# Kernel optimization log

Measured on AMD Instinct MI355X. Metric: run time of the kernel, lower is better.

Reference implementation:

```python
import jax, jax.numpy as jnp
import numpy as np

B, S, D, H, KS, VS, O = 4, 2048, 1024, 16, 64, 64, 1024


def setup_inputs() -> dict:
    key = jax.random.key(0)
    ks = jax.random.split(key, 11)
    def w(k, shp):
        return jax.random.normal(k, shp, dtype=jnp.float32) * 0.02
    return {
        "Q": jax.random.normal(ks[0], (B, S, D), dtype=jnp.float32),
        "K": jax.random.normal(ks[1], (B, S, D), dtype=jnp.float32),
        "V": jax.random.normal(ks[2], (B, S, D), dtype=jnp.float32),
        # per-head projection weights stacked over heads (equivalent to 3*H separate nn.Linear)
        "Wq": w(ks[3], (H, D, KS)), "bq": w(ks[4], (H, KS)),
        "Wk": w(ks[5], (H, D, KS)), "bk": w(ks[6], (H, KS)),
        "Wv": w(ks[7], (H, D, VS)), "bv": w(ks[8], (H, VS)),
        "Wo": w(ks[9], (H * VS, O)), "bo": w(ks[10], (O,)),
    }


def reference(Q, K, V, Wq, bq, Wk, bk, Wv, bv, Wo, bo):
    scale = jnp.sqrt(jnp.asarray(KS, dtype=Q.dtype))
    # per-head linear projections (vectorized over heads)
    q = jnp.einsum('bsd,hdk->bhsk', Q, Wq) + bq[:, None, :]   # [B,H,S,KS]
    k = jnp.einsum('bsd,hdk->bhsk', K, Wk) + bk[:, None, :]   # [B,H,S,KS]
    v = jnp.einsum('bsd,hdv->bhsv', V, Wv) + bv[:, None, :]   # [B,H,S,VS]
    # scaled dot-product attention, full S x S scores per head
    scores = jnp.einsum('bhsk,bhtk->bhst', q, k) / scale       # [B,H,S,S]
    attn = jax.nn.softmax(scores, axis=-1)
    heads = jnp.einsum('bhst,bhtv->bhsv', attn, v)             # [B,H,S,VS]
    # concat heads along feature dim -> [B,S,H*VS]
    cat = jnp.transpose(heads, (0, 2, 1, 3)).reshape(B, S, H * VS)
    return cat @ Wo + bo
```

## Files before the change

kernel.cpp:

```cpp
#include <hip/hip_runtime.h>
#include <hip/hip_fp16.h>
#include <cstdint>
#include <cstddef>

typedef _Float16 f16;
typedef _Float16 f16x8 __attribute__((ext_vector_type(8)));
typedef _Float16 f16x4 __attribute__((ext_vector_type(4)));
typedef float    f32x4 __attribute__((ext_vector_type(4)));

#define MFMA(a, b, c) __builtin_amdgcn_mfma_f32_16x16x32_f16(a, b, c, 0, 0, 0)


__device__ __forceinline__ void gload_lds16(const f16* g, f16* l) {
    __builtin_amdgcn_global_load_lds(
        (const __attribute__((address_space(1))) void*)g,
        (__attribute__((address_space(3))) void*)l, 16, 0, 0);
}

__global__ void k_transpose_all(const float* __restrict__ Wq, const float* __restrict__ Wk,
                                const float* __restrict__ Wv, const float* __restrict__ Wo,
                                f16* __restrict__ WT, f16* __restrict__ WoT) {
    __shared__ float T[64][65];
    const int bx = blockIdx.x;
    const int widx = bx >> 8, sub = bx & 255;
    const int nb = sub >> 4, db = sub & 15;
    const int tid = threadIdx.x;
    const float* W = widx == 0 ? Wq : (widx == 1 ? Wk : (widx == 2 ? Wv : Wo));
    f16* Wt = (widx < 3) ? (WT + (size_t)widx * 1048576) : WoT;
    const float* src = (widx < 3) ? (W + nb * 65536 + db * 4096)
                                  : (W + db * 65536 + nb * 64);
    const int rstride = (widx < 3) ? 64 : 1024;
    {
        int nn = tid & 63, d0 = tid >> 6;
#pragma unroll
        for (int p = 0; p < 16; ++p) {
            int dd = p * 4 + d0;
            T[dd][nn] = src[dd * rstride + nn];
        }
    }
    __syncthreads();
    {
        int dd = tid & 63, n0 = tid >> 6;
#pragma unroll
        for (int p = 0; p < 16; ++p) {
            int nn = p * 4 + n0;
            Wt[(size_t)(nb * 64 + nn) * 1024 + db * 64 + dd] = (f16)T[dd][nn];
        }
    }
}

#define G256_STAGE(AD, BD, ASRC, BSRC, KT)                                      \
    do {                                                                        \
        int ktc = (KT);                                                         \
        _Pragma("unroll")                                                       \
        for (int i2 = 0; i2 < 4; ++i2) {                                        \
            int gA = wid * 4 + i2;                                              \
            gload_lds16(&(ASRC)[(size_t)(row0 + gA * 8 + (lane >> 3)) * 1024    \
                                + ktc * 64 + (lane & 7) * 8],                   \
                        &(AD)[(gA * 68 + lane) * 8]);                           \
        }                                                                       \
        _Pragma("unroll")                                                       \
        for (int i2 = 0; i2 < 2; ++i2) {                                        \
            int gB = wid * 2 + i2;                                              \
            gload_lds16(&(BSRC)[(size_t)(col0 + gB * 8 + (lane >> 3)) * 1024    \
                                + ktc * 64 + (lane & 7) * 8],                   \
                        &(BD)[(gB * 68 + lane) * 8]);                           \
        }                                                                       \
    } while (0)

#define G256_STAGE_B(BD, BSRC, KT)                                             \
    do {                                                                        \
        int ktc = (KT);                                                         \
        _Pragma("unroll")                                                       \
        for (int i2 = 0; i2 < 2; ++i2) {                                        \
            int gB = wid * 2 + i2;                                              \
            gload_lds16(&(BSRC)[(size_t)(col0 + gB * 8 + (lane >> 3)) * 1024    \
                                + ktc * 64 + (lane & 7) * 8],                   \
                        &(BD)[(gB * 68 + lane) * 8]);                           \
        }                                                                       \
    } while (0)

#define QKV_ISSUE_A(KT)                                                         \
    do {                                                                        \
        int ktc = (KT);                                                         \
        _Pragma("unroll")                                                       \
        for (int i2 = 0; i2 < 4; ++i2) {                                        \
            int gA = wid * 4 + i2;                                              \
            const float* p = &Af[(size_t)(row0 + gA * 8 + (lane >> 3)) * 1024   \
                                 + ktc * 64 + (lane & 7) * 8];                  \
            alo[i2] = *(const float4*)p;                                        \
            ahi[i2] = *(const float4*)(p + 4);                                  \
        }                                                                       \
    } while (0)

#define QKV_WRITE_A(AD)                                                         \
    do {                                                                        \
        _Pragma("unroll")                                                       \
        for (int i2 = 0; i2 < 4; ++i2) {                                        \
            int gA = wid * 4 + i2;                                              \
            union { uint32_t u[4]; f16x8 v; } hh;                               \
            hh.u[0] = __builtin_bit_cast(uint32_t,                              \
                        __builtin_amdgcn_cvt_pkrtz(alo[i2].x, alo[i2].y));      \
            hh.u[1] = __builtin_bit_cast(uint32_t,                              \
                        __builtin_amdgcn_cvt_pkrtz(alo[i2].z, alo[i2].w));      \
            hh.u[2] = __builtin_bit_cast(uint32_t,                              \
                        __builtin_amdgcn_cvt_pkrtz(ahi[i2].x, ahi[i2].y));      \
            hh.u[3] = __builtin_bit_cast(uint32_t,                              \
                        __builtin_amdgcn_cvt_pkrtz(ahi[i2].z, ahi[i2].w));      \
            *(f16x8*)&(AD)[(gA * 68 + lane) * 8] = hh.v;                        \
        }                                                                       \
    } while (0)

#define G256_COMPUTE(AB, BB)                                                    \
    do {                                                                        \
        _Pragma("unroll")                                                       \
        for (int kk = 0; kk < 2; ++kk) {                                        \
            f16x8 af[4], bf[4];                                                 \
            _Pragma("unroll")                                                   \
            for (int m = 0; m < 4; ++m) {                                       \
                int rw = wm * 64 + m * 16 + lr;                                 \
                af[m] = *(const f16x8*)&(AB)[((rw >> 3) * 68 + (rw & 7) * 8     \
                                              + kk * 4 + lg) * 8];              \
            }                                                                   \
            _Pragma("unroll")                                                   \
            for (int n = 0; n < 4; ++n) {                                       \
                int rw = wn * 64 + n * 16 + lr;                                 \
                bf[n] = *(const f16x8*)&(BB)[((rw >> 3) * 68 + (rw & 7) * 8     \
                                              + kk * 4 + lg) * 8];              \
            }                                                                   \
            _Pragma("unroll")                                                   \
            for (int m = 0; m < 4; ++m)                                         \
                _Pragma("unroll")                                               \
                for (int n = 0; n < 4; ++n)                                     \
                    acc[m][n] = MFMA(af[m], bf[n], acc[m][n]);                  \
        }                                                                       \
    } while (0)

#define G256_PIPELINE(ASRC, BSRC)                                              \
    int cur = 0, nx1 = 1, nx2 = 2;                                             \
    G256_STAGE(As3, Bs3, ASRC, BSRC, 0);                                       \
    for (int t = 0; t < 16; ++t) {                                             \
        int tn = t < 15 ? t + 1 : 15;                                          \
        G256_STAGE(As3 + nx1 * 17408, Bs3 + nx1 * 8704, ASRC, BSRC, tn);       \
        asm volatile("s_waitcnt vmcnt(6)" ::: "memory");                       \
        __builtin_amdgcn_sched_barrier(0);                                     \
        __builtin_amdgcn_s_barrier();                                          \
        __builtin_amdgcn_sched_barrier(0);                                     \
        const f16* Ab = As3 + cur * 17408;                                     \
        const f16* Bb = Bs3 + cur * 8704;                                      \
        G256_COMPUTE(Ab, Bb);                                                  \
        int tmp = cur; cur = nx1; nx1 = nx2; nx2 = tmp;                        \
    }

__global__ __launch_bounds__(512, 1) void k_gemm_qkv256(
    const float* __restrict__ Qf, const float* __restrict__ Kf, const float* __restrict__ Vf,
    const f16* __restrict__ WT, const float* __restrict__ bq,
    const float* __restrict__ bk, const float* __restrict__ bv,
    f16* __restrict__ qout, f16* __restrict__ kout, f16* __restrict__ vout, float SC) {
    __shared__ f16 As3[3 * 17408];
    __shared__ f16 Bs3[3 * 8704];
    const int yy = blockIdx.y;
    const int seg = yy >> 3;
    const float* Af = seg == 0 ? Qf : (seg == 1 ? Kf : Vf);
    const f16* Bt   = WT + (size_t)seg * 1048576;
    const float* bias = seg == 0 ? bq : (seg == 1 ? bk : bv);
    const float scale = seg == 0 ? SC : 1.0f;

    const int tid = threadIdx.x;
    const int wid = tid >> 6, lane = tid & 63;
    const int wm = wid >> 1, wn = wid & 1;
    const int lr = lane & 15, lg = lane >> 4;
    const int row0 = blockIdx.x * 256, col0 = (yy & 7) * 128;

    f32x4 acc[4][4];
#pragma unroll
    for (int m = 0; m < 4; ++m)
#pragma unroll
        for (int n = 0; n < 4; ++n) acc[m][n] = (f32x4){0.f, 0.f, 0.f, 0.f};

    float4 alo[4], ahi[4];

    G256_STAGE_B(Bs3, Bt, 0);
    QKV_ISSUE_A(0);
    asm volatile("s_waitcnt vmcnt(0)" ::: "memory");
    QKV_WRITE_A(As3);
    G256_STAGE_B(Bs3 + 8704, Bt, 1);
    QKV_ISSUE_A(1);
    asm volatile("s_waitcnt lgkmcnt(0)" ::: "memory");
    __builtin_amdgcn_sched_barrier(0);
    __builtin_amdgcn_s_barrier();
    __builtin_amdgcn_sched_barrier(0);

    int cur = 0, nx1 = 1, nx2 = 2;
    for (int t = 0; t < 16; ++t) {
        const f16* Ab = As3 + cur * 17408;
        const f16* Bb = Bs3 + cur * 8704;
        G256_COMPUTE(Ab, Bb);
        int tn2 = t + 2 <= 15 ? t + 2 : 15;
        asm volatile("s_waitcnt vmcnt(0)" ::: "memory");
        __builtin_amdgcn_sched_barrier(0);
        QKV_WRITE_A(As3 + nx1 * 17408);
        G256_STAGE_B(Bs3 + nx2 * 8704, Bt, tn2);
        QKV_ISSUE_A(tn2);
        asm volatile("s_waitcnt lgkmcnt(0)" ::: "memory");
        __builtin_amdgcn_sched_barrier(0);
        __builtin_amdgcn_s_barrier();
        __builtin_amdgcn_sched_barrier(0);
        int tmp = cur; cur = nx1; nx1 = nx2; nx2 = tmp;
    }

#pragma unroll
    for (int m = 0; m < 4; ++m) {
#pragma unroll
        for (int n = 0; n < 4; ++n) {
            int col = col0 + wn * 64 + n * 16 + lr;
            float bv_ = bias[col];
            int rowb = row0 + wm * 64 + m * 16 + lg * 4;
            int srow = rowb & 2047;
            if (seg == 0) {
#pragma unroll
                for (int r = 0; r < 4; ++r) {
                    int row = rowb + r;
                    size_t a = ((size_t)((row >> 11) * 16 + (col >> 6)) * 2048 + (row & 2047)) * 64 + (col & 63);
                    qout[a] = (f16)((acc[m][n][r] + bv_) * scale);
                }
            } else if (seg == 1) {
                int ks5 = srow & 31;
                int p0 = ((ks5 >> 2) & 1) * 16 + (ks5 >> 3) * 4 + (ks5 & 3);
                size_t abase = (size_t)((rowb >> 11) * 16 + (col >> 6)) * 131072
                             + (size_t)(srow >> 5) * 2048
                             + (size_t)(p0 >> 4) * 512
                             + (size_t)((col & 63) >> 5) * 1024
                             + (size_t)((col & 31) >> 3) * 128
                             + (col & 7);
#pragma unroll
                for (int r = 0; r < 4; ++r)
                    kout[abase + (size_t)((p0 & 15) + r) * 8] = (f16)(acc[m][n][r] + bv_);
            } else {
                size_t a = (size_t)((rowb >> 11) * 16 + (col >> 6)) * 131072
                         + (size_t)(srow >> 5) * 2048
                         + (size_t)((col & 63) >> 4) * 512
                         + (size_t)((srow & 31) >> 3) * 128
                         + (size_t)(col & 15) * 8
                         + (srow & 7);
                f16x4 ov;
#pragma unroll
                for (int r = 0; r < 4; ++r) ov[r] = (f16)(acc[m][n][r] + bv_);
                *(f16x4*)&vout[a] = ov;
            }
        }
    }
}

__global__ __launch_bounds__(512, 1) void k_gemm_out256(const f16* __restrict__ A,
                                                        const f16* __restrict__ Bt,
                                                        const float* __restrict__ bias,
                                                        float* __restrict__ Cout) {
    __shared__ f16 As3[3 * 17408];
    __shared__ f16 Bs3[3 * 8704];
    const int tid = threadIdx.x;
    const int wid = tid >> 6, lane = tid & 63;
    const int wm = wid >> 1, wn = wid & 1;
    const int lr = lane & 15, lg = lane >> 4;
    const int row0 = blockIdx.x * 256, col0 = blockIdx.y * 128;

    f32x4 acc[4][4];
#pragma unroll
    for (int m = 0; m < 4; ++m)
#pragma unroll
        for (int n = 0; n < 4; ++n) acc[m][n] = (f32x4){0.f, 0.f, 0.f, 0.f};

    G256_PIPELINE(A, Bt)

#pragma unroll
    for (int m = 0; m < 4; ++m) {
#pragma unroll
        for (int n = 0; n < 4; ++n) {
            int col = col0 + wn * 64 + n * 16 + lr;
            float bv = bias[col];
#pragma unroll
            for (int r = 0; r < 4; ++r) {
                int row = row0 + wm * 64 + m * 16 + lg * 4 + r;
                Cout[(size_t)row * 1024 + col] = acc[m][n][r] + bv;
            }
        }
    }
}

#define ATTN_TILE(Kc, Vc)                                                     \
    do {                                                                      \
        f16x8 ka0 = *(const f16x8*)&(Kc)[fo];                                 \
        f16x8 ka1 = *(const f16x8*)&(Kc)[fo + 1024];                          \
        f16x8 ka2 = *(const f16x8*)&(Kc)[fo + 512];                           \
        f16x8 ka3 = *(const f16x8*)&(Kc)[fo + 1536];                          \
        f32x4 st[2][2];                                                       \
        __builtin_amdgcn_s_setprio(1);                                        \
        _Pragma("unroll")                                                     \
        for (int qt = 0; qt < 2; ++qt) {                                      \
            float nm = -m_r[qt];                                              \
            f32x4 z = (f32x4){nm, nm, nm, nm};                                \
            z = MFMA(ka0, qf[qt][0], z);                                      \
            z = MFMA(ka1, qf[qt][1], z);                                      \
            st[qt][0] = z;                                                    \
            f32x4 z2 = (f32x4){nm, nm, nm, nm};                               \
            z2 = MFMA(ka2, qf[qt][0], z2);                                    \
            z2 = MFMA(ka3, qf[qt][1], z2);                                    \
            st[qt][1] = z2;                                                   \
        }                                                                     \
        __builtin_amdgcn_s_setprio(0);                                        \
        f16x8 vv0 = *(const f16x8*)&(Vc)[fo];                                 \
        f16x8 vv1 = *(const f16x8*)&(Vc)[fo + 512];                           \
        f16x8 vv2 = *(const f16x8*)&(Vc)[fo + 1024];                          \
        f16x8 vv3 = *(const f16x8*)&(Vc)[fo + 1536];                          \
        {                                                                     \
            float lm[2];                                                      \
            _Pragma("unroll")                                                 \
            for (int qt = 0; qt < 2; ++qt) {                                  \
                float a0 = fmaxf(fmaxf(st[qt][0][0], st[qt][0][1]), st[qt][0][2]); \
                float b0 = fmaxf(fmaxf(st[qt][0][3], st[qt][1][0]), st[qt][1][1]); \
                float c0 = fmaxf(fmaxf(st[qt][1][2], st[qt][1][3]), a0);      \
                lm[qt] = fmaxf(b0, c0);                                       \
            }                                                                 \
            if (__any((lm[0] > THR) || (lm[1] > THR))) {                      \
                _Pragma("unroll")                                             \
                for (int qt = 0; qt < 2; ++qt) {                              \
                    float t0v = lm[qt];                                       \
                    t0v = fmaxf(t0v, __shfl_xor(t0v, 16, 64));                \
                    t0v = fmaxf(t0v, __shfl_xor(t0v, 32, 64));                \
                    float delta = fmaxf(0.f, t0v);                            \
                    float alpha = __builtin_amdgcn_exp2f(-delta);             \
                    _Pragma("unroll")                                         \
                    for (int m = 0; m < 4; ++m)                               \
                        _Pragma("unroll")                                     \
                        for (int r = 0; r < 4; ++r) o[qt][m][r] *= alpha;     \
                    _Pragma("unroll")                                         \
                    for (int r = 0; r < 4; ++r) ol[qt][r] *= alpha;           \
                    m_r[qt] += delta;                                         \
                    _Pragma("unroll")                                         \
                    for (int t = 0; t < 2; ++t)                               \
                        _Pragma("unroll")                                     \
                        for (int r = 0; r < 4; ++r) st[qt][t][r] -= delta;    \
                }                                                             \
            }                                                                 \
        }                                                                     \
        f16x8 pf[2];                                                          \
        _Pragma("unroll")                                                     \
        for (int qt = 0; qt < 2; ++qt) {                                      \
            union { uint32_t u[4]; f16x8 v; } bb;                             \
            _Pragma("unroll")                                                 \
            for (int t = 0; t < 2; ++t)                                       \
                _Pragma("unroll")                                             \
                for (int pr = 0; pr < 2; ++pr) {                              \
                    float e0 = __builtin_amdgcn_exp2f(st[qt][t][2 * pr]);     \
                    float e1 = __builtin_amdgcn_exp2f(st[qt][t][2 * pr + 1]); \
                    auto hp = __builtin_amdgcn_cvt_pkrtz(e0, e1);             \
                    bb.u[t * 2 + pr] = __builtin_bit_cast(uint32_t, hp);      \
                }                                                             \
            pf[qt] = bb.v;                                                    \
        }                                                                     \
        __builtin_amdgcn_s_setprio(1);                                        \
        _Pragma("unroll")                                                     \
        for (int qt = 0; qt < 2; ++qt) {                                      \
            o[qt][0] = MFMA(vv0, pf[qt], o[qt][0]);                           \
            o[qt][1] = MFMA(vv1, pf[qt], o[qt][1]);                           \
            o[qt][2] = MFMA(vv2, pf[qt], o[qt][2]);                           \
            o[qt][3] = MFMA(vv3, pf[qt], o[qt][3]);                           \
            ol[qt]   = MFMA(ones, pf[qt], ol[qt]);                            \
        }                                                                     \
        __builtin_amdgcn_s_setprio(0);                                        \
    } while (0)

__global__ __launch_bounds__(512, 4) void k_attn(const f16* __restrict__ q,
                                                 const f16* __restrict__ k2,
                                                 const f16* __restrict__ v2,
                                                 f16* __restrict__ cat) {
    const int g = blockIdx.x;
    const int xcd = g & 7, i = g >> 3;
    const int bh = xcd * 8 + (i >> 3);
    const int qb = i & 7;
    const int b = bh >> 4, h = bh & 15;

    const int tid = threadIdx.x, wid = tid >> 6, lane = tid & 63;
    const int lr = lane & 15, lg = lane >> 4;
    const int qw = qb * 256 + wid * 32;

    __shared__ f16 Ks[4][2048];
    __shared__ f16 Vs[4][2048];

    const float THR = 8.0f;

    f16x8 qf[2][2];
#pragma unroll
    for (int qt = 0; qt < 2; ++qt)
#pragma unroll
        for (int hf = 0; hf < 2; ++hf)
            qf[qt][hf] = *(const f16x8*)&q[((size_t)bh * 2048 + qw + qt * 16 + lr) * 64 + hf * 32 + lg * 8];

    const f16* kt = k2 + (size_t)bh * 131072;
    const f16* vt = v2 + (size_t)bh * 131072;
    const bool sgK = (tid < 256);
    const int so2 = (tid & 255) * 8;
    const int fo = lane * 8;

    f16x8 ones;
#pragma unroll
    for (int j = 0; j < 8; ++j) ones[j] = (f16)1.0f;

    f32x4 o[2][4], ol[2];
#pragma unroll
    for (int qt = 0; qt < 2; ++qt) {
#pragma unroll
        for (int m = 0; m < 4; ++m) o[qt][m] = (f32x4){0.f, 0.f, 0.f, 0.f};
        ol[qt] = (f32x4){0.f, 0.f, 0.f, 0.f};
    }
    float m_r[2] = {0.f, 0.f};

    if (sgK) {
        gload_lds16(kt + so2, &Ks[0][so2]);
        gload_lds16(kt + 2048 + so2, &Ks[1][so2]);
    } else {
        gload_lds16(vt + so2, &Vs[0][so2]);
        gload_lds16(vt + 2048 + so2, &Vs[1][so2]);
    }
    __syncthreads();

    const bool rev = (wid & 1);
    for (int pp = 0; pp < 32; ++pp) {
        const int t0 = 2 * pp;
        const int ba = t0 & 3, bb2 = (t0 + 1) & 3;
        const int bc = (t0 + 2) & 3, bd = (t0 + 3) & 3;

        if (sgK) {
            gload_lds16(kt + (size_t)(t0 + 2) * 2048 + so2, &Ks[bc][so2]);
            gload_lds16(kt + (size_t)(t0 + 3) * 2048 + so2, &Ks[bd][so2]);
        } else {
            gload_lds16(vt + (size_t)(t0 + 2) * 2048 + so2, &Vs[bc][so2]);
            gload_lds16(vt + (size_t)(t0 + 3) * 2048 + so2, &Vs[bd][so2]);
        }

        if (rev) {
            ATTN_TILE(&Ks[bb2][0], &Vs[bb2][0]);
            ATTN_TILE(&Ks[ba][0], &Vs[ba][0]);
        } else {
            ATTN_TILE(&Ks[ba][0], &Vs[ba][0]);
            ATTN_TILE(&Ks[bb2][0], &Vs[bb2][0]);
        }

        __syncthreads();
    }

#pragma unroll
    for (int qt = 0; qt < 2; ++qt) {
        float inv = 1.f / ol[qt][0];
        size_t cb = ((size_t)b * 2048 + qw + qt * 16 + lr) * 1024 + h * 64 + lg * 4;
#pragma unroll
        for (int m = 0; m < 4; ++m) {
            f16x4 ov;
#pragma unroll
            for (int r = 0; r < 4; ++r) ov[r] = (f16)(o[qt][m][r] * inv);
            *(f16x4*)&cat[cb + m * 16] = ov;
        }
    }
}

extern "C" void kernel_launch(void* const* d_in, const int* in_sizes, int n_in,
                              void* d_out, int out_size, void* d_ws, size_t ws_size,
                              hipStream_t stream) {
    const float* Q  = (const float*)d_in[0];
    const float* K  = (const float*)d_in[1];
    const float* V  = (const float*)d_in[2];
    const float* Wq = (const float*)d_in[3];
    const float* bq = (const float*)d_in[4];
    const float* Wk = (const float*)d_in[5];
    const float* bk = (const float*)d_in[6];
    const float* Wv = (const float*)d_in[7];
    const float* bv = (const float*)d_in[8];
    const float* Wo = (const float*)d_in[9];
    const float* bo = (const float*)d_in[10];

    char* ws = (char*)d_ws;
    size_t off = 0;
    auto alloc = [&](size_t bytes) {
        char* p = ws + off;
        off += (bytes + 255) & ~(size_t)255;
        return p;
    };
    f16* WT  = (f16*)alloc(3ULL * 1024 * 1024 * 2);
    f16* WoT = (f16*)alloc(1024ULL * 1024 * 2);
    f16* qb  = (f16*)alloc(8192ULL * 1024 * 2);
    f16* kb2 = (f16*)alloc(8192ULL * 1024 * 2);
    f16* vb2 = (f16*)alloc(8192ULL * 1024 * 2);
    f16* cat = (f16*)alloc(8192ULL * 1024 * 2);

    k_transpose_all<<<1024, 256, 0, stream>>>(Wq, Wk, Wv, Wo, WT, WoT);

    const float SC = 0.125f * 1.44269504089f;
    k_gemm_qkv256<<<dim3(32, 24), 512, 0, stream>>>(Q, K, V, WT, bq, bk, bv,
                                                    qb, kb2, vb2, SC);

    k_attn<<<512, 512, 0, stream>>>(qb, kb2, vb2, cat);

    k_gemm_out256<<<dim3(32, 8), 512, 0, stream>>>(cat, WoT, bo, (float*)d_out);
}
```

Baseline: 183.4 us.

## Double-buffer A registers in QKV GEMM to keep loads in flight

Restructures the QKV projection main loop into a two-step unrolled pipeline with two register sets for the fp32 A tile. Each step issues the next tile's global loads, then uses a partial vmcnt wait so only the older loads must finish before converting and writing the current A tile to LDS. The previous loop waited on vmcnt(0) every iteration. The change aims to hide global load latency behind LDS writes and MFMA compute, at the cost of extra VGPRs for the second A buffer, which may lower occupancy. It also depends on the hand-counted vmcnt value being correct.

```diff
diff --git a/kernel.cpp b/kernel.cpp
--- a/kernel.cpp
+++ b/kernel.cpp
@@ -80,7 +80,7 @@
         }                                                                       \
     } while (0)
 
-#define QKV_ISSUE_A(KT)                                                         \
+#define QKV_ISSUE_A(ALO, AHI, KT)                                               \
     do {                                                                        \
         int ktc = (KT);                                                         \
         _Pragma("unroll")                                                       \
@@ -88,25 +88,25 @@
             int gA = wid * 4 + i2;                                              \
             const float* p = &Af[(size_t)(row0 + gA * 8 + (lane >> 3)) * 1024   \
                                  + ktc * 64 + (lane & 7) * 8];                  \
-            alo[i2] = *(const float4*)p;                                        \
-            ahi[i2] = *(const float4*)(p + 4);                                  \
+            ALO[i2] = *(const float4*)p;                                        \
+            AHI[i2] = *(const float4*)(p + 4);                                  \
         }                                                                       \
     } while (0)
 
-#define QKV_WRITE_A(AD)                                                         \
+#define QKV_WRITE_A(AD, ALO, AHI)                                               \
     do {                                                                        \
         _Pragma("unroll")                                                       \
         for (int i2 = 0; i2 < 4; ++i2) {                                        \
             int gA = wid * 4 + i2;                                              \
             union { uint32_t u[4]; f16x8 v; } hh;                               \
             hh.u[0] = __builtin_bit_cast(uint32_t,                              \
-                        __builtin_amdgcn_cvt_pkrtz(alo[i2].x, alo[i2].y));      \
+                        __builtin_amdgcn_cvt_pkrtz(ALO[i2].x, ALO[i2].y));      \
             hh.u[1] = __builtin_bit_cast(uint32_t,                              \
-                        __builtin_amdgcn_cvt_pkrtz(alo[i2].z, alo[i2].w));      \
+                        __builtin_amdgcn_cvt_pkrtz(ALO[i2].z, ALO[i2].w));      \
             hh.u[2] = __builtin_bit_cast(uint32_t,                              \
-                        __builtin_amdgcn_cvt_pkrtz(ahi[i2].x, ahi[i2].y));      \
+                        __builtin_amdgcn_cvt_pkrtz(AHI[i2].x, AHI[i2].y));      \
             hh.u[3] = __builtin_bit_cast(uint32_t,                              \
-                        __builtin_amdgcn_cvt_pkrtz(ahi[i2].z, ahi[i2].w));      \
+                        __builtin_amdgcn_cvt_pkrtz(AHI[i2].z, AHI[i2].w));      \
             *(f16x8*)&(AD)[(gA * 68 + lane) * 8] = hh.v;                        \
         }                                                                       \
     } while (0)
@@ -178,35 +178,45 @@
 #pragma unroll
         for (int n = 0; n < 4; ++n) acc[m][n] = (f32x4){0.f, 0.f, 0.f, 0.f};
 
-    float4 alo[4], ahi[4];
+    float4 aloA[4], ahiA[4], aloB[4], ahiB[4];
 
     G256_STAGE_B(Bs3, Bt, 0);
-    QKV_ISSUE_A(0);
-    asm volatile("s_waitcnt vmcnt(0)" ::: "memory");
-    QKV_WRITE_A(As3);
-    G256_STAGE_B(Bs3 + 8704, Bt, 1);
-    QKV_ISSUE_A(1);
-    asm volatile("s_waitcnt lgkmcnt(0)" ::: "memory");
-    __builtin_amdgcn_sched_barrier(0);
-    __builtin_amdgcn_s_barrier();
-    __builtin_amdgcn_sched_barrier(0);
+    QKV_ISSUE_A(aloA, ahiA, 0);
 
     int cur = 0, nx1 = 1, nx2 = 2;
-    for (int t = 0; t < 16; ++t) {
-        const f16* Ab = As3 + cur * 17408;
-        const f16* Bb = Bs3 + cur * 8704;
-        G256_COMPUTE(Ab, Bb);
-        int tn2 = t + 2 <= 15 ? t + 2 : 15;
-        asm volatile("s_waitcnt vmcnt(0)" ::: "memory");
-        __builtin_amdgcn_sched_barrier(0);
-        QKV_WRITE_A(As3 + nx1 * 17408);
-        G256_STAGE_B(Bs3 + nx2 * 8704, Bt, tn2);
-        QKV_ISSUE_A(tn2);
-        asm volatile("s_waitcnt lgkmcnt(0)" ::: "memory");
-        __builtin_amdgcn_sched_barrier(0);
-        __builtin_amdgcn_s_barrier();
-        __builtin_amdgcn_sched_barrier(0);
-        int tmp = cur; cur = nx1; nx1 = nx2; nx2 = tmp;
+    for (int tp = 0; tp < 8; ++tp) {
+        const int t0 = 2 * tp;
+        {
+            G256_STAGE_B(Bs3 + nx1 * 8704, Bt, t0 + 1);
+            QKV_ISSUE_A(aloB, ahiB, t0 + 1);
+            asm volatile("s_waitcnt vmcnt(10)" ::: "memory");
+            __builtin_amdgcn_sched_barrier(0);
+            QKV_WRITE_A(As3 + cur * 17408, aloA, ahiA);
+            asm volatile("s_waitcnt lgkmcnt(0)" ::: "memory");
+            __builtin_amdgcn_sched_barrier(0);
+            __builtin_amdgcn_s_barrier();
+            __builtin_amdgcn_sched_barrier(0);
+            G256_COMPUTE(As3 + cur * 17408, Bs3 + cur * 8704);
+            int tmp = cur; cur = nx1; nx1 = nx2; nx2 = tmp;
+        }
+        {
+            const int t1 = t0 + 1;
+            if (t1 < 15) {
+                G256_STAGE_B(Bs3 + nx1 * 8704, Bt, t1 + 1);
+                QKV_ISSUE_A(aloA, ahiA, t1 + 1);
+                asm volatile("s_waitcnt vmcnt(10)" ::: "memory");
+            } else {
+                asm volatile("s_waitcnt vmcnt(0)" ::: "memory");
+            }
+            __builtin_amdgcn_sched_barrier(0);
+            QKV_WRITE_A(As3 + cur * 17408, aloB, ahiB);
+            asm volatile("s_waitcnt lgkmcnt(0)" ::: "memory");
+            __builtin_amdgcn_sched_barrier(0);
+            __builtin_amdgcn_s_barrier();
+            __builtin_amdgcn_sched_barrier(0);
+            G256_COMPUTE(As3 + cur * 17408, Bs3 + cur * 8704);
+            int tmp = cur; cur = nx1; nx1 = nx2; nx2 = tmp;
+        }
     }
 
 #pragma unroll
```

Measured after the change: 185.5 us. About the same (+1.2%).
